# Optimization experiments

Measured on AMD Instinct MI355X. Metric: run time of the kernel, lower is better.

The kernel has to match this reference:

```python
import jax, jax.numpy as jnp
import numpy as np

B, N, DIM = 2, 8192, 3
K = 16            # num_neighbours (dilation=1)
R = 2048          # num_representitives
CIN, CL, COUT = 64, 16, 128
K2 = K * K


def _bn(x, g, b):
    # BatchNorm in eval mode with running_mean=0, running_var=1 -> affine
    return x * g + b


def setup_inputs() -> dict:
    key = jax.random.key(0)
    ks = jax.random.split(key, 24)
    r = lambda i, shape, s=1.0: jax.random.normal(ks[i], shape, jnp.float32) * s
    return {
        "points": r(0, (B, N, DIM)),
        "features": r(1, (B, N, CIN)),
        "lift_w": r(2, (CL, DIM), 0.3), "lift_b": r(3, (CL,), 0.1),
        "bn_lift_g": 1.0 + r(4, (CL,), 0.1), "bn_lift_b": r(5, (CL,), 0.1),
        "t1_w": r(6, (K2, DIM * K), 0.1), "t1_b": r(7, (K2,), 0.1),
        "bn1_g": 1.0 + r(8, (K2,), 0.1), "bn1_b": r(9, (K2,), 0.1),
        "t2_w": r(10, (K2, K2), 0.05), "t2_b": r(11, (K2,), 0.1),
        "bn2_g": 1.0 + r(12, (K2,), 0.1), "bn2_b": r(13, (K2,), 0.1),
        "t3_w": r(14, (K2, K2), 0.05), "t3_b": r(15, (K2,), 0.1),
        "bn3_g": 1.0 + r(16, (K2,), 0.1), "bn3_b": r(17, (K2,), 0.1),
        "conv_w": r(18, (COUT, CIN + CL, K), 0.05), "conv_b": r(19, (COUT,), 0.1),
        "rep_idx": jax.random.permutation(ks[20], N)[:R],
    }


def reference(points, features, lift_w, lift_b, bn_lift_g, bn_lift_b,
              t1_w, t1_b, bn1_g, bn1_b, t2_w, t2_b, bn2_g, bn2_b,
              t3_w, t3_b, bn3_g, bn3_b, conv_w, conv_b, rep_idx):
    b, n, _ = points.shape
    # ---- KNN (squared distance is order-equivalent to torch.cdist) ----
    sq = jnp.sum(points * points, -1)                                   # (b,n)
    d2 = sq[:, :, None] + sq[:, None, :] - 2.0 * jnp.einsum('bnd,bmd->bnm', points, points)
    _, idx = jax.lax.top_k(-d2, K + 1)                                  # (b,n,K+1)
    nn_idx = idx[:, :, 1:]                                              # drop self
    # ---- representative sampling + neighbor gather ----
    rep_pos = points[:, rep_idx]                                        # (b,R,3)
    nb_idx = nn_idx[:, rep_idx]                                         # (b,R,K)
    gather = jax.vmap(lambda arr, i: arr[i])
    nbr_pos = gather(points, nb_idx)                                    # (b,R,K,3)
    nbr_feat = gather(features, nb_idx)                                 # (b,R,K,CIN)
    # ---- X_conv ----
    p = (nbr_pos - rep_pos[:, :, None, :]).reshape(b * R, K, DIM)       # centered
    lifted = jax.nn.relu(_bn(p @ lift_w.T + lift_b, bn_lift_g, bn_lift_b))  # (bR,K,CL)
    feat = jnp.concatenate([lifted, nbr_feat.reshape(b * R, K, CIN)], -1)   # (bR,K,CL+CIN)
    pf = p.reshape(b * R, K * DIM)
    h = jax.nn.relu(_bn(pf @ t1_w.T + t1_b, bn1_g, bn1_b))
    h = jax.nn.relu(_bn(h @ t2_w.T + t2_b, bn2_g, bn2_b))
    T = _bn(h @ t3_w.T + t3_b, bn3_g, bn3_b).reshape(b * R, K, K)       # learned transform
    Tf = jnp.einsum('bij,bjc->bic', T, feat)                            # bmm, (bR,K,C)
    # Conv1d(C, COUT, kernel=K) over length K -> single output position
    out = jnp.einsum('bkc,ock->bo', Tf, conv_w) + conv_b                # (bR,COUT)
    return rep_pos, out.reshape(b, R, COUT)
```

## Files before the change

### kernel.cpp

```cpp
#include <hip/hip_runtime.h>
#include <float.h>

#define Bn 2
#define Nn 8192
#define Rr 2048
#define Kk 16
#define CIN 64
#define CL 16
#define COUT 128
#define K2c 256
#define GT (Bn*Rr)
#define FD (CL+CIN)
#define KC (Kk*FD)
#define MG 8

__global__ __launch_bounds__(256) void prep_kernel(
    const float* __restrict__ t1_w, const float* __restrict__ t2_w,
    const float* __restrict__ t3_w, const float* __restrict__ conv_w,
    const float* __restrict__ points,
    float* __restrict__ t1t, float* __restrict__ t2t,
    float* __restrict__ t3t, float* __restrict__ wp,
    float4* __restrict__ pts4)
{
  int i = blockIdx.x * 256 + threadIdx.x;
  if (i < K2c*48) { int j = i / 48, k = i - j*48; t1t[k*K2c + j] = t1_w[i]; }
  if (i < K2c*K2c) { int j = i >> 8, k = i & 255; t2t[k*K2c + j] = t2_w[i]; t3t[k*K2c + j] = t3_w[i]; }
  if (i < COUT*KC) {
    int o = i / KC, ck = i - o*KC;
    int c = ck >> 4, k = ck & 15;
    wp[(k*FD + c)*COUT + o] = conv_w[i];
  }
  if (i < Bn*Nn) {
    float x = points[i*3+0], y = points[i*3+1], z = points[i*3+2];
    float sq = __fadd_rn(__fadd_rn(__fmul_rn(x,x), __fmul_rn(y,y)), __fmul_rn(z,z));
    pts4[i] = make_float4(x, y, z, sq);
  }
}

__global__ __launch_bounds__(512) void knn_kernel(
    const float4* __restrict__ pts4, const int* __restrict__ rep_idx,
    int* __restrict__ nb_idx, float* __restrict__ p_out,
    float* __restrict__ rep_pos_out)
{
  __shared__ float4 ptsS[3072];
  __shared__ unsigned long long coll[8][128];
  int t    = threadIdx.x;
  int lane = t & 63;
  int w    = t >> 6;
  int g    = blockIdx.x * 8 + w;
  int b    = g >> 11;
  int r    = g & 2047;
  int n    = rep_idx[r];
  const float4* pb4 = pts4 + (size_t)b*Nn;
  float4 Q = pb4[n];
  float qx = Q.x, qy = Q.y, qz = Q.z, sqn = Q.w;

  float c0 = FLT_MAX, c1 = FLT_MAX, c2 = FLT_MAX;
  for (int c = 0; c < 3; c++) {
    int base  = c * 3072;
    int count = (c < 2) ? 3072 : 2048;
    __syncthreads();
    for (int i = t; i < count; i += 512) ptsS[i] = pb4[base + i];
    __syncthreads();
    int iters = count >> 6;
    #pragma unroll 4
    for (int j = 0; j < iters; j++) {
      float4 P = ptsS[j*64 + lane];
      float dot = __fmaf_rn(qz, P.z, __fmaf_rn(qy, P.y, __fmul_rn(qx, P.x)));
      float d2  = __fsub_rn(__fadd_rn(sqn, P.w), __fmul_rn(2.0f, dot));
      float nc2 = __builtin_amdgcn_fmed3f(c1, c2, d2);
      float nc1 = __builtin_amdgcn_fmed3f(c0, c1, d2);
      float nc0 = fminf(c0, d2);
      c0 = nc0; c1 = nc1; c2 = nc2;
    }
  }

  float tau = FLT_MAX;
  for (int rnd = 0; rnd < 17; rnd++) {
    float m = c0;
    #pragma unroll
    for (int off = 1; off < 64; off <<= 1) m = fminf(m, __shfl_xor(m, off));
    if (c0 == m) { c0 = c1; c1 = c2; c2 = FLT_MAX; }
    tau = m;
  }

  int cnt = 0;
  for (int c = 0; c < 3; c++) {
    int base  = c * 3072;
    int count = (c < 2) ? 3072 : 2048;
    __syncthreads();
    for (int i = t; i < count; i += 512) ptsS[i] = pb4[base + i];
    __syncthreads();
    int iters = count >> 6;
    #pragma unroll 4
    for (int j = 0; j < iters; j++) {
      float4 P = ptsS[j*64 + lane];
      float dot = __fmaf_rn(qz, P.z, __fmaf_rn(qy, P.y, __fmul_rn(qx, P.x)));
      float d2  = __fsub_rn(__fadd_rn(sqn, P.w), __fmul_rn(2.0f, dot));
      bool pr = (d2 <= tau);
      unsigned long long mask = __ballot(pr);
      if (pr) {
        int pos = cnt + (int)__popcll(mask & ((1ull << lane) - 1ull));
        if (pos < 128) {
          unsigned f = __float_as_uint(d2);
          unsigned mono = f ^ ((unsigned)((int)f >> 31) | 0x80000000u);
          coll[w][pos] = ((unsigned long long)mono << 32) | (unsigned)(base + j*64 + lane);
        }
      }
      cnt += (int)__popcll(mask);
    }
  }
  if (cnt > 128) cnt = 128;

  unsigned long long e1 = (lane < cnt)      ? coll[w][lane]      : ~0ull;
  unsigned long long e2 = (lane + 64 < cnt) ? coll[w][lane + 64] : ~0ull;
  int out_m = 0;
  for (int rnd = 0; rnd < 17; rnd++) {
    unsigned long long myk = (e1 < e2) ? e1 : e2;
    unsigned long long kmin = myk;
    #pragma unroll
    for (int off = 1; off < 64; off <<= 1) {
      unsigned long long o = __shfl_xor(kmin, off);
      kmin = (o < kmin) ? o : kmin;
    }
    if (rnd >= 1 && lane == rnd - 1) out_m = (int)(kmin & 0xFFFFFFFFull);
    if (kmin == e1) e1 = ~0ull;
    else if (kmin == e2) e2 = ~0ull;
  }

  if (lane < 16) {
    nb_idx[g*Kk + lane] = out_m;
    float4 P = pb4[out_m];
    p_out[(g*Kk + lane)*3 + 0] = __fsub_rn(P.x, qx);
    p_out[(g*Kk + lane)*3 + 1] = __fsub_rn(P.y, qy);
    p_out[(g*Kk + lane)*3 + 2] = __fsub_rn(P.z, qz);
  }
  if (lane < 3) rep_pos_out[g*3 + lane] = (lane == 0 ? qx : (lane == 1 ? qy : qz));
}

__device__ __forceinline__ void fma_g(float4& a, float hv, const float4& wv) {
  a.x = fmaf(hv, wv.x, a.x);
  a.y = fmaf(hv, wv.y, a.y);
  a.z = fmaf(hv, wv.z, a.z);
  a.w = fmaf(hv, wv.w, a.w);
}

__global__ __launch_bounds__(256) void mlp_kernel(
    const float* __restrict__ p,
    const float* __restrict__ t1t, const float* __restrict__ t1_b,
    const float* __restrict__ g1v, const float* __restrict__ b1v,
    const float* __restrict__ t2t, const float* __restrict__ t2_b,
    const float* __restrict__ g2v, const float* __restrict__ b2v,
    const float* __restrict__ t3t, const float* __restrict__ t3_b,
    const float* __restrict__ g3v, const float* __restrict__ b3v,
    float* __restrict__ T_out)
{
  __shared__ float pf[48][MG];
  __shared__ float hA[K2c][MG];
  __shared__ float red[4][64][36];
  int t = threadIdx.x;
  int w = t >> 6, l = t & 63;
  int g0 = blockIdx.x * MG;
  for (int e = t; e < MG*48; e += 256) {
    int g = e / 48, k = e - g*48;
    pf[k][g] = p[(size_t)(g0+g)*48 + k];
  }
  __syncthreads();

  float4 acc[8];

#define KLOOP(WSRC, KDIM, HBUF)                                        \
  {                                                                    \
    _Pragma("unroll")                                                  \
    for (int q = 0; q < 8; q++) acc[q] = make_float4(0.f,0.f,0.f,0.f); \
    float4 wb0 = *(const float4*)&WSRC[(size_t)w*K2c + 4*l];           \
    float4 wb1 = (w + 4 < KDIM) ?                                      \
        *(const float4*)&WSRC[(size_t)(w+4)*K2c + 4*l] : wb0;          \
    _Pragma("unroll 2")                                                \
    for (int k = w; k < KDIM; k += 4) {                                \
      float4 wc = wb0; wb0 = wb1;                                      \
      if (k + 8 < KDIM)                                                \
        wb1 = *(const float4*)&WSRC[(size_t)(k+8)*K2c + 4*l];          \
      float4 h0 = *(const float4*)&HBUF[k][0];                         \
      float4 h1 = *(const float4*)&HBUF[k][4];                         \
      fma_g(acc[0], h0.x, wc); fma_g(acc[1], h0.y, wc);                \
      fma_g(acc[2], h0.z, wc); fma_g(acc[3], h0.w, wc);                \
      fma_g(acc[4], h1.x, wc); fma_g(acc[5], h1.y, wc);                \
      fma_g(acc[6], h1.z, wc); fma_g(acc[7], h1.w, wc);                \
    }                                                                  \
  }

#define WRITE_RED()                                                        \
  {                                                                        \
    float4 ra, rb;                                                         \
    ra = make_float4(acc[0].x, acc[1].x, acc[2].x, acc[3].x);              \
    rb = make_float4(acc[4].x, acc[5].x, acc[6].x, acc[7].x);              \
    *(float4*)&red[w][l][0]  = ra; *(float4*)&red[w][l][4]  = rb;          \
    ra = make_float4(acc[0].y, acc[1].y, acc[2].y, acc[3].y);              \
    rb = make_float4(acc[4].y, acc[5].y, acc[6].y, acc[7].y);              \
    *(float4*)&red[w][l][8]  = ra; *(float4*)&red[w][l][12] = rb;          \
    ra = make_float4(acc[0].z, acc[1].z, acc[2].z, acc[3].z);              \
    rb = make_float4(acc[4].z, acc[5].z, acc[6].z, acc[7].z);              \
    *(float4*)&red[w][l][16] = ra; *(float4*)&red[w][l][20] = rb;          \
    ra = make_float4(acc[0].w, acc[1].w, acc[2].w, acc[3].w);              \
    rb = make_float4(acc[4].w, acc[5].w, acc[6].w, acc[7].w);              \
    *(float4*)&red[w][l][24] = ra; *(float4*)&red[w][l][28] = rb;          \
  }

#define REDUCE(SA, SB)                                                     \
  float4 SA = make_float4(0.f,0.f,0.f,0.f), SB = SA;                       \
  {                                                                        \
    int lr = t >> 2, cc = t & 3;                                           \
    _Pragma("unroll")                                                      \
    for (int ww = 0; ww < 4; ww++) {                                       \
      float4 pa = *(const float4*)&red[ww][lr][cc*8 + 0];                  \
      float4 pb = *(const float4*)&red[ww][lr][cc*8 + 4];                  \
      SA.x += pa.x; SA.y += pa.y; SA.z += pa.z; SA.w += pa.w;              \
      SB.x += pb.x; SB.y += pb.y; SB.z += pb.z; SB.w += pb.w;              \
    }                                                                      \
  }

  KLOOP(t1t, 48, pf)
  WRITE_RED()
  __syncthreads();
  {
    REDUCE(sa, sb)
    float bb = t1_b[t], gg = g1v[t], oo = b1v[t];
    float4 va, vb;
    va.x = fmaxf(fmaf(sa.x + bb, gg, oo), 0.f);
    va.y = fmaxf(fmaf(sa.y + bb, gg, oo), 0.f);
    va.z = fmaxf(fmaf(sa.z + bb, gg, oo), 0.f);
    va.w = fmaxf(fmaf(sa.w + bb, gg, oo), 0.f);
    vb.x = fmaxf(fmaf(sb.x + bb, gg, oo), 0.f);
    vb.y = fmaxf(fmaf(sb.y + bb, gg, oo), 0.f);
    vb.z = fmaxf(fmaf(sb.z + bb, gg, oo), 0.f);
    vb.w = fmaxf(fmaf(sb.w + bb, gg, oo), 0.f);
    *(float4*)&hA[t][0] = va;
    *(float4*)&hA[t][4] = vb;
  }
  __syncthreads();

  KLOOP(t2t, K2c, hA)
  __syncthreads();
  WRITE_RED()
  __syncthreads();
  {
    REDUCE(sa, sb)
    float bb = t2_b[t], gg = g2v[t], oo = b2v[t];
    float4 va, vb;
    va.x = fmaxf(fmaf(sa.x + bb, gg, oo), 0.f);
    va.y = fmaxf(fmaf(sa.y + bb, gg, oo), 0.f);
    va.z = fmaxf(fmaf(sa.z + bb, gg, oo), 0.f);
    va.w = fmaxf(fmaf(sa.w + bb, gg, oo), 0.f);
    vb.x = fmaxf(fmaf(sb.x + bb, gg, oo), 0.f);
    vb.y = fmaxf(fmaf(sb.y + bb, gg, oo), 0.f);
    vb.z = fmaxf(fmaf(sb.z + bb, gg, oo), 0.f);
    vb.w = fmaxf(fmaf(sb.w + bb, gg, oo), 0.f);
    *(float4*)&hA[t][0] = va;
    *(float4*)&hA[t][4] = vb;
  }
  __syncthreads();

  KLOOP(t3t, K2c, hA)
  WRITE_RED()
  __syncthreads();
  {
    REDUCE(sa, sb)
    float bb = t3_b[t], gg = g3v[t], oo = b3v[t];
    T_out[(size_t)(g0+0)*K2c + t] = fmaf(sa.x + bb, gg, oo);
    T_out[(size_t)(g0+1)*K2c + t] = fmaf(sa.y + bb, gg, oo);
    T_out[(size_t)(g0+2)*K2c + t] = fmaf(sa.z + bb, gg, oo);
    T_out[(size_t)(g0+3)*K2c + t] = fmaf(sa.w + bb, gg, oo);
    T_out[(size_t)(g0+4)*K2c + t] = fmaf(sb.x + bb, gg, oo);
    T_out[(size_t)(g0+5)*K2c + t] = fmaf(sb.y + bb, gg, oo);
    T_out[(size_t)(g0+6)*K2c + t] = fmaf(sb.z + bb, gg, oo);
    T_out[(size_t)(g0+7)*K2c + t] = fmaf(sb.w + bb, gg, oo);
  }
#undef KLOOP
#undef WRITE_RED
#undef REDUCE
}

__global__ __launch_bounds__(256) void tf_kernel(
    const float* __restrict__ T_in, const float* __restrict__ features,
    const float* __restrict__ p, const int* __restrict__ nb_idx,
    const float* __restrict__ lift_w, const float* __restrict__ lift_b,
    const float* __restrict__ bng, const float* __restrict__ bnb,
    float* __restrict__ Tf)
{
  __shared__ float T_s[4*K2c];
  __shared__ float f_s[4*KC];
  __shared__ float ps[4*48];
  __shared__ int   idxs[64];
  __shared__ float lw[48], lb2[16], lg[16], lo[16];
  int t = threadIdx.x;
  int g0 = blockIdx.x * 4;
  int b = g0 / Rr;
  for (int e = t; e < 4*K2c; e += 256) T_s[e] = T_in[(size_t)g0*K2c + e];
  if (t >= 32 && t < 224) {
    int e = t - 32;
    ps[e] = p[(size_t)g0*48 + e];
  }
  if (t < 16) ps[176 + t] = p[(size_t)g0*48 + 176 + t];
  if (t < 64) idxs[t] = nb_idx[g0*16 + t];
  if (t >= 64 && t < 112)  lw[t-64]   = lift_w[t-64];
  if (t >= 112 && t < 128) lb2[t-112] = lift_b[t-112];
  if (t >= 224 && t < 240) lg[t-224]  = bng[t-224];
  if (t >= 240)            lo[t-240]  = bnb[t-240];
  __syncthreads();

  {
    int wv = t >> 6, ln = t & 63;
    for (int row = wv; row < 64; row += 4) {
      int gg = row >> 4, k = row & 15;
      f_s[gg*KC + k*FD + CL + ln] = features[((size_t)b*Nn + idxs[row])*CIN + ln];
    }
  }
  for (int e = t; e < 1024; e += 256) {
    int gg = e >> 8, rem = e & 255, k = rem >> 4, c = rem & 15;
    float acc = ps[gg*48 + k*3 + 0]*lw[c*3+0] + ps[gg*48 + k*3 + 1]*lw[c*3+1]
              + ps[gg*48 + k*3 + 2]*lw[c*3+2] + lb2[c];
    acc = acc*lg[c] + lo[c];
    f_s[gg*KC + k*FD + c] = fmaxf(acc, 0.f);
  }
  __syncthreads();

  int gg = t >> 6;
  int cl = t & 63;
  for (int ci = cl; ci < FD; ci += 64) {
    float fcol[16];
    #pragma unroll
    for (int j = 0; j < 16; j++) fcol[j] = f_s[gg*KC + j*FD + ci];
    #pragma unroll
    for (int k = 0; k < 16; k++) {
      float acc = 0.f;
      #pragma unroll
      for (int j = 0; j < 16; j++) acc = fmaf(T_s[gg*K2c + k*16 + j], fcol[j], acc);
      Tf[(size_t)(g0+gg)*KC + k*FD + ci] = acc;
    }
  }
}

__global__ __launch_bounds__(256) void gemm_kernel(
    const float* __restrict__ A,
    const float* __restrict__ Bm,
    float* __restrict__ part)
{
  __shared__ float As[16*36];
  __shared__ float Bs[16*COUT];
  int t = threadIdx.x;
  int m0 = blockIdx.x * 32;
  int ky = blockIdx.y;
  int kbase0 = ky * (KC/8);
  float acc[4][4];
  #pragma unroll
  for (int i = 0; i < 4; i++)
    #pragma unroll
    for (int j = 0; j < 4; j++) acc[i][j] = 0.f;
  int tn = t & 31, tm = t >> 5;

  for (int kt = 0; kt < KC/8; kt += 16) {
    int kb = kbase0 + kt;
    {
      int kcol = t & 15, row = t >> 4;
      As[kcol*36 + row]      = A[(size_t)(m0+row)*KC + kb + kcol];
      As[kcol*36 + row + 16] = A[(size_t)(m0+row+16)*KC + kb + kcol];
    }
    {
      int o = t & 127, kk2 = t >> 7;
      #pragma unroll
      for (int p4 = 0; p4 < 8; p4++) {
        int kk = kk2 + p4*2;
        Bs[kk*COUT + o] = Bm[(size_t)(kb+kk)*COUT + o];
      }
    }
    __syncthreads();
    #pragma unroll
    for (int kk = 0; kk < 16; kk++) {
      float4 a4 = *(const float4*)&As[kk*36 + tm*4];
      float4 b4 = *(const float4*)&Bs[kk*COUT + tn*4];
      float av[4] = {a4.x, a4.y, a4.z, a4.w};
      float bv[4] = {b4.x, b4.y, b4.z, b4.w};
      #pragma unroll
      for (int i = 0; i < 4; i++)
        #pragma unroll
        for (int j = 0; j < 4; j++) acc[i][j] = fmaf(av[i], bv[j], acc[i][j]);
    }
    __syncthreads();
  }
  #pragma unroll
  for (int i = 0; i < 4; i++) {
    float4 v = make_float4(acc[i][0], acc[i][1], acc[i][2], acc[i][3]);
    *(float4*)&part[((size_t)ky*GT + m0 + tm*4 + i)*COUT + tn*4] = v;
  }
}

__global__ __launch_bounds__(256) void reduce_kernel(
    const float* __restrict__ part, const float* __restrict__ conv_b,
    float* __restrict__ outp)
{
  int i = blockIdx.x*256 + threadIdx.x;
  float4 s = ((const float4*)conv_b)[i & 31];
  #pragma unroll
  for (int w = 0; w < 8; w++) {
    float4 v = ((const float4*)(part + (size_t)w*GT*COUT))[i];
    s.x += v.x; s.y += v.y; s.z += v.z; s.w += v.w;
  }
  ((float4*)outp)[i] = s;
}

extern "C" void kernel_launch(void* const* d_in, const int* in_sizes, int n_in,
                              void* d_out, int out_size, void* d_ws, size_t ws_size,
                              hipStream_t stream) {
  const float* points   = (const float*)d_in[0];
  const float* features = (const float*)d_in[1];
  const float* lift_w   = (const float*)d_in[2];
  const float* lift_b   = (const float*)d_in[3];
  const float* bn_lift_g= (const float*)d_in[4];
  const float* bn_lift_b= (const float*)d_in[5];
  const float* t1_w     = (const float*)d_in[6];
  const float* t1_b     = (const float*)d_in[7];
  const float* bn1_g    = (const float*)d_in[8];
  const float* bn1_b    = (const float*)d_in[9];
  const float* t2_w     = (const float*)d_in[10];
  const float* t2_b     = (const float*)d_in[11];
  const float* bn2_g    = (const float*)d_in[12];
  const float* bn2_b    = (const float*)d_in[13];
  const float* t3_w     = (const float*)d_in[14];
  const float* t3_b     = (const float*)d_in[15];
  const float* bn3_g    = (const float*)d_in[16];
  const float* bn3_b    = (const float*)d_in[17];
  const float* conv_w   = (const float*)d_in[18];
  const float* conv_b   = (const float*)d_in[19];
  const int*   rep_idx  = (const int*)d_in[20];

  char* ws = (char*)d_ws;
  int*    nb   = (int*)   (ws + 0);
  float*  p    = (float*) (ws + 262144);
  float*  T    = (float*) (ws + 1048576);
  float*  Tf   = (float*) (ws + 5242880);
  float*  wp   = (float*) (ws + 26214400);
  float*  t1t  = (float*) (ws + 26869760);
  float*  t2t  = (float*) (ws + 26918912);
  float*  t3t  = (float*) (ws + 27181056);
  float*  part = (float*) (ws + 33554432);
  float4* pts4 = (float4*)(ws + 52428800);

  float* rep_pos = (float*)d_out;
  float* outp    = (float*)d_out + (size_t)GT*3;

  prep_kernel<<<640, 256, 0, stream>>>(t1_w, t2_w, t3_w, conv_w, points,
                                       t1t, t2t, t3t, wp, pts4);
  knn_kernel<<<GT/8, 512, 0, stream>>>(pts4, rep_idx, nb, p, rep_pos);
  mlp_kernel<<<GT/MG, 256, 0, stream>>>(p, t1t, t1_b, bn1_g, bn1_b,
                                        t2t, t2_b, bn2_g, bn2_b,
                                        t3t, t3_b, bn3_g, bn3_b, T);
  tf_kernel<<<GT/4, 256, 0, stream>>>(T, features, p, nb,
                                      lift_w, lift_b, bn_lift_g, bn_lift_b, Tf);
  dim3 ggrid(GT/32, 8);
  gemm_kernel<<<ggrid, 256, 0, stream>>>(Tf, wp, part);
  reduce_kernel<<<(GT*COUT/4)/256, 256, 0, stream>>>(part, conv_b, outp);
}
```

Measured before the change: 225.3 us.

## Shrink MLP group size, cheapen KNN threshold search, reuse resident point chunk

The MLP kernel now handles 4 representatives per block instead of 8. This halves the accumulators per thread and gives twice as many blocks. Its reduction scratch becomes a padded scalar layout, and one redundant barrier is removed. The KNN threshold is now taken from each lane's third-smallest candidate over 6 shuffle rounds instead of 17. That bound is looser but still valid, since it covers at least 18 points. The second pass starts with the chunk still held in shared memory, which saves one reload. A redundant load of the tail of the shared position buffer is also dropped. The looser threshold may collect more candidates, and the smaller MLP groups reload weights more often.

```diff
diff --git a/kernel.cpp b/kernel.cpp
--- a/kernel.cpp
+++ b/kernel.cpp
@@ -12,7 +12,7 @@
 #define GT (Bn*Rr)
 #define FD (CL+CIN)
 #define KC (Kk*FD)
-#define MG 8
+#define MG 4
 
 __global__ __launch_bounds__(256) void prep_kernel(
     const float* __restrict__ t1_w, const float* __restrict__ t2_w,
@@ -76,21 +76,25 @@
   }
 
   float tau = FLT_MAX;
-  for (int rnd = 0; rnd < 17; rnd++) {
-    float m = c0;
+  for (int rnd = 0; rnd < 6; rnd++) {
+    float m = c2;
     #pragma unroll
     for (int off = 1; off < 64; off <<= 1) m = fminf(m, __shfl_xor(m, off));
-    if (c0 == m) { c0 = c1; c1 = c2; c2 = FLT_MAX; }
+    if (c2 == m) c2 = FLT_MAX;
     tau = m;
   }
 
   int cnt = 0;
-  for (int c = 0; c < 3; c++) {
+  #pragma unroll
+  for (int cc = 0; cc < 3; cc++) {
+    int c = (cc == 0) ? 2 : (cc - 1);
     int base  = c * 3072;
     int count = (c < 2) ? 3072 : 2048;
-    __syncthreads();
-    for (int i = t; i < count; i += 512) ptsS[i] = pb4[base + i];
-    __syncthreads();
+    if (cc != 0) {
+      __syncthreads();
+      for (int i = t; i < count; i += 512) ptsS[i] = pb4[base + i];
+      __syncthreads();
+    }
     int iters = count >> 6;
     #pragma unroll 4
     for (int j = 0; j < iters; j++) {
@@ -157,7 +161,7 @@
 {
   __shared__ float pf[48][MG];
   __shared__ float hA[K2c][MG];
-  __shared__ float red[4][64][36];
+  __shared__ float red[4*16*66];
   int t = threadIdx.x;
   int w = t >> 6, l = t & 63;
   int g0 = blockIdx.x * MG;
@@ -167,12 +171,12 @@
   }
   __syncthreads();
 
-  float4 acc[8];
+  float4 acc[MG];
 
 #define KLOOP(WSRC, KDIM, HBUF)                                        \
   {                                                                    \
     _Pragma("unroll")                                                  \
-    for (int q = 0; q < 8; q++) acc[q] = make_float4(0.f,0.f,0.f,0.f); \
+    for (int q = 0; q < MG; q++) acc[q] = make_float4(0.f,0.f,0.f,0.f);\
     float4 wb0 = *(const float4*)&WSRC[(size_t)w*K2c + 4*l];           \
     float4 wb1 = (w + 4 < KDIM) ?                                      \
         *(const float4*)&WSRC[(size_t)(w+4)*K2c + 4*l] : wb0;          \
@@ -181,83 +185,63 @@
       float4 wc = wb0; wb0 = wb1;                                      \
       if (k + 8 < KDIM)                                                \
         wb1 = *(const float4*)&WSRC[(size_t)(k+8)*K2c + 4*l];          \
-      float4 h0 = *(const float4*)&HBUF[k][0];                         \
-      float4 h1 = *(const float4*)&HBUF[k][4];                         \
-      fma_g(acc[0], h0.x, wc); fma_g(acc[1], h0.y, wc);                \
-      fma_g(acc[2], h0.z, wc); fma_g(acc[3], h0.w, wc);                \
-      fma_g(acc[4], h1.x, wc); fma_g(acc[5], h1.y, wc);                \
-      fma_g(acc[6], h1.z, wc); fma_g(acc[7], h1.w, wc);                \
+      float4 h = *(const float4*)&HBUF[k][0];                          \
+      fma_g(acc[0], h.x, wc); fma_g(acc[1], h.y, wc);                  \
+      fma_g(acc[2], h.z, wc); fma_g(acc[3], h.w, wc);                  \
     }                                                                  \
   }
 
-#define WRITE_RED()                                                        \
-  {                                                                        \
-    float4 ra, rb;                                                         \
-    ra = make_float4(acc[0].x, acc[1].x, acc[2].x, acc[3].x);              \
-    rb = make_float4(acc[4].x, acc[5].x, acc[6].x, acc[7].x);              \
-    *(float4*)&red[w][l][0]  = ra; *(float4*)&red[w][l][4]  = rb;          \
-    ra = make_float4(acc[0].y, acc[1].y, acc[2].y, acc[3].y);              \
-    rb = make_float4(acc[4].y, acc[5].y, acc[6].y, acc[7].y);              \
-    *(float4*)&red[w][l][8]  = ra; *(float4*)&red[w][l][12] = rb;          \
-    ra = make_float4(acc[0].z, acc[1].z, acc[2].z, acc[3].z);              \
-    rb = make_float4(acc[4].z, acc[5].z, acc[6].z, acc[7].z);              \
-    *(float4*)&red[w][l][16] = ra; *(float4*)&red[w][l][20] = rb;          \
-    ra = make_float4(acc[0].w, acc[1].w, acc[2].w, acc[3].w);              \
-    rb = make_float4(acc[4].w, acc[5].w, acc[6].w, acc[7].w);              \
-    *(float4*)&red[w][l][24] = ra; *(float4*)&red[w][l][28] = rb;          \
-  }
-
-#define REDUCE(SA, SB)                                                     \
-  float4 SA = make_float4(0.f,0.f,0.f,0.f), SB = SA;                       \
-  {                                                                        \
-    int lr = t >> 2, cc = t & 3;                                           \
-    _Pragma("unroll")                                                      \
-    for (int ww = 0; ww < 4; ww++) {                                       \
-      float4 pa = *(const float4*)&red[ww][lr][cc*8 + 0];                  \
-      float4 pb = *(const float4*)&red[ww][lr][cc*8 + 4];                  \
-      SA.x += pa.x; SA.y += pa.y; SA.z += pa.z; SA.w += pa.w;              \
-      SB.x += pb.x; SB.y += pb.y; SB.z += pb.z; SB.w += pb.w;              \
-    }                                                                      \
+#define WRITE_RED()                                                    \
+  {                                                                    \
+    _Pragma("unroll")                                                  \
+    for (int q = 0; q < MG; q++) {                                     \
+      red[(w*16 + 0*4 + q)*66 + l] = acc[q].x;                         \
+      red[(w*16 + 1*4 + q)*66 + l] = acc[q].y;                         \
+      red[(w*16 + 2*4 + q)*66 + l] = acc[q].z;                         \
+      red[(w*16 + 3*4 + q)*66 + l] = acc[q].w;                         \
+    }                                                                  \
+  }
+
+#define REDUCE(S)                                                      \
+  float4 S = make_float4(0.f,0.f,0.f,0.f);                             \
+  {                                                                    \
+    int lr = t >> 2, cc = t & 3;                                       \
+    _Pragma("unroll")                                                  \
+    for (int ww = 0; ww < 4; ww++) {                                   \
+      S.x += red[(ww*16 + cc*4 + 0)*66 + lr];                          \
+      S.y += red[(ww*16 + cc*4 + 1)*66 + lr];                          \
+      S.z += red[(ww*16 + cc*4 + 2)*66 + lr];                          \
+      S.w += red[(ww*16 + cc*4 + 3)*66 + lr];                          \
+    }                                                                  \
   }
 
   KLOOP(t1t, 48, pf)
   WRITE_RED()
   __syncthreads();
   {
-    REDUCE(sa, sb)
+    REDUCE(s)
     float bb = t1_b[t], gg = g1v[t], oo = b1v[t];
-    float4 va, vb;
-    va.x = fmaxf(fmaf(sa.x + bb, gg, oo), 0.f);
-    va.y = fmaxf(fmaf(sa.y + bb, gg, oo), 0.f);
-    va.z = fmaxf(fmaf(sa.z + bb, gg, oo), 0.f);
-    va.w = fmaxf(fmaf(sa.w + bb, gg, oo), 0.f);
-    vb.x = fmaxf(fmaf(sb.x + bb, gg, oo), 0.f);
-    vb.y = fmaxf(fmaf(sb.y + bb, gg, oo), 0.f);
-    vb.z = fmaxf(fmaf(sb.z + bb, gg, oo), 0.f);
-    vb.w = fmaxf(fmaf(sb.w + bb, gg, oo), 0.f);
-    *(float4*)&hA[t][0] = va;
-    *(float4*)&hA[t][4] = vb;
+    float4 v;
+    v.x = fmaxf(fmaf(s.x + bb, gg, oo), 0.f);
+    v.y = fmaxf(fmaf(s.y + bb, gg, oo), 0.f);
+    v.z = fmaxf(fmaf(s.z + bb, gg, oo), 0.f);
+    v.w = fmaxf(fmaf(s.w + bb, gg, oo), 0.f);
+    *(float4*)&hA[t][0] = v;
   }
   __syncthreads();
 
   KLOOP(t2t, K2c, hA)
-  __syncthreads();
   WRITE_RED()
   __syncthreads();
   {
-    REDUCE(sa, sb)
+    REDUCE(s)
     float bb = t2_b[t], gg = g2v[t], oo = b2v[t];
-    float4 va, vb;
-    va.x = fmaxf(fmaf(sa.x + bb, gg, oo), 0.f);
-    va.y = fmaxf(fmaf(sa.y + bb, gg, oo), 0.f);
-    va.z = fmaxf(fmaf(sa.z + bb, gg, oo), 0.f);
-    va.w = fmaxf(fmaf(sa.w + bb, gg, oo), 0.f);
-    vb.x = fmaxf(fmaf(sb.x + bb, gg, oo), 0.f);
-    vb.y = fmaxf(fmaf(sb.y + bb, gg, oo), 0.f);
-    vb.z = fmaxf(fmaf(sb.z + bb, gg, oo), 0.f);
-    vb.w = fmaxf(fmaf(sb.w + bb, gg, oo), 0.f);
-    *(float4*)&hA[t][0] = va;
-    *(float4*)&hA[t][4] = vb;
+    float4 v;
+    v.x = fmaxf(fmaf(s.x + bb, gg, oo), 0.f);
+    v.y = fmaxf(fmaf(s.y + bb, gg, oo), 0.f);
+    v.z = fmaxf(fmaf(s.z + bb, gg, oo), 0.f);
+    v.w = fmaxf(fmaf(s.w + bb, gg, oo), 0.f);
+    *(float4*)&hA[t][0] = v;
   }
   __syncthreads();
 
@@ -265,16 +249,12 @@
   WRITE_RED()
   __syncthreads();
   {
-    REDUCE(sa, sb)
+    REDUCE(s)
     float bb = t3_b[t], gg = g3v[t], oo = b3v[t];
-    T_out[(size_t)(g0+0)*K2c + t] = fmaf(sa.x + bb, gg, oo);
-    T_out[(size_t)(g0+1)*K2c + t] = fmaf(sa.y + bb, gg, oo);
-    T_out[(size_t)(g0+2)*K2c + t] = fmaf(sa.z + bb, gg, oo);
-    T_out[(size_t)(g0+3)*K2c + t] = fmaf(sa.w + bb, gg, oo);
-    T_out[(size_t)(g0+4)*K2c + t] = fmaf(sb.x + bb, gg, oo);
-    T_out[(size_t)(g0+5)*K2c + t] = fmaf(sb.y + bb, gg, oo);
-    T_out[(size_t)(g0+6)*K2c + t] = fmaf(sb.z + bb, gg, oo);
-    T_out[(size_t)(g0+7)*K2c + t] = fmaf(sb.w + bb, gg, oo);
+    T_out[(size_t)(g0+0)*K2c + t] = fmaf(s.x + bb, gg, oo);
+    T_out[(size_t)(g0+1)*K2c + t] = fmaf(s.y + bb, gg, oo);
+    T_out[(size_t)(g0+2)*K2c + t] = fmaf(s.z + bb, gg, oo);
+    T_out[(size_t)(g0+3)*K2c + t] = fmaf(s.w + bb, gg, oo);
   }
 #undef KLOOP
 #undef WRITE_RED
@@ -301,7 +281,6 @@
     int e = t - 32;
     ps[e] = p[(size_t)g0*48 + e];
   }
-  if (t < 16) ps[176 + t] = p[(size_t)g0*48 + 176 + t];
   if (t < 64) idxs[t] = nb_idx[g0*16 + t];
   if (t >= 64 && t < 112)  lw[t-64]   = lift_w[t-64];
   if (t >= 112 && t < 128) lb2[t-112] = lift_b[t-112];
```

After: 222.6 us. About the same (-1.2%).
